# Performance work log

Hardware: AMD Instinct MI355X
Metric: run time of the kernel (lower is better)

Reference implementation:

```python
import jax, jax.numpy as jnp
import numpy as np

N = 50000      # batch_node_num (unique nodes)
E = 800000     # number of edges (avg degree 16)
IN = 128       # in_dim
OUT = 128      # out_dim
B = 10000      # query nodes


def setup_inputs() -> dict:
    key = jax.random.key(0)
    k = jax.random.split(key, 8)
    edges = jax.random.randint(k[0], (E, 2), 0, N, dtype=jnp.int64)
    node_idx = jax.random.randint(k[1], (B,), 0, N, dtype=jnp.int64)
    local_features = jax.random.normal(k[2], (N, IN), dtype=jnp.float32)
    W1 = jax.random.normal(k[3], (IN, OUT), dtype=jnp.float32) * (1.0 / np.sqrt(IN))
    b1 = jnp.zeros((OUT,), dtype=jnp.float32)
    W2 = jax.random.normal(k[4], (OUT, OUT), dtype=jnp.float32) * (1.0 / np.sqrt(OUT))
    b2 = jnp.zeros((OUT,), dtype=jnp.float32)
    return {"edges": edges, "node_idx": node_idx, "local_features": local_features,
            "W1": W1, "b1": b1, "W2": W2, "b2": b2, "ind": 2}


def reference(edges, node_idx, local_features, W1, b1, W2, b2, ind):
    mask = jnp.array([1.0, 1.0, 0.0, 0.0], dtype=jnp.float32)
    # Linear -> Tanh -> Linear (the out_linear_layer MLP)
    h = jnp.tanh(local_features @ W1 + b1) @ W2 + b2          # [N, OUT]
    src, dst = edges[:, 0], edges[:, 1]
    # self-loop edges get weight mask[ind], others weight 1
    values = jnp.where(src == dst, mask[ind], jnp.float32(1.0))  # [E]
    # spmm(matrix, ones) == per-row degree (weighted)
    row_sum = jax.ops.segment_sum(values, src, num_segments=N)   # [N]
    row_sum = jnp.where(row_sum == 0, jnp.float32(1.0), row_sum)
    # spmm(matrix, new_embeddings): gather dst embeddings, scatter-add to src
    results = jax.ops.segment_sum(values[:, None] * h[dst], src, num_segments=N)  # [N, OUT]
    output_emb = results / row_sum[:, None]
    return output_emb[node_idx]
```

## Files before the change

kernel.cpp:

```cpp
#include <hip/hip_runtime.h>

#define IN_DIM 128
#define CAP 128
#define LDT 136
#define SCAT_BLOCKS 384

typedef short v8s __attribute__((ext_vector_type(8)));
typedef float v4f __attribute__((ext_vector_type(4)));

__device__ inline unsigned short f2bf(float f) {
    unsigned int u = __float_as_uint(f);
    u += 0x7FFFu + ((u >> 16) & 1u);
    return (unsigned short)(u >> 16);
}
__device__ inline float bf2f(unsigned short h) {
    return __uint_as_float((unsigned int)h << 16);
}

__global__ __launch_bounds__(256) void prep(
    const float* __restrict__ W1, const float* __restrict__ W2,
    unsigned short* __restrict__ Wt1, unsigned short* __restrict__ Wt2,
    const int* __restrict__ node_idx, int* __restrict__ flag, int B,
    int* __restrict__ cursor, int N, int nbF)
{
    int bid = blockIdx.x;
    if (bid < 128) {
        int i = bid * 256 + threadIdx.x;
        int m = i >> 14, rem = i & 16383;
        int n = rem >> 7, k = rem & 127;
        float wv = (m ? W2 : W1)[k * 128 + n];
        int half = k >> 6, ch = (k >> 3) & 7, k0 = k & 7;
        int idx = half * 8192 + n * 64 + ((ch ^ (n & 7)) << 3) + k0;
        (m ? Wt2 : Wt1)[idx] = f2bf(wv);
    } else if (bid < 128 + nbF) {
        int i = (bid - 128) * 256 + threadIdx.x;
        if (i < B) flag[node_idx[i]] = 1;
    } else {
        int i = (bid - 128 - nbF) * 256 + threadIdx.x;
        if (i < N) cursor[i] = 0;
    }
}

__global__ __launch_bounds__(256, 3) void mlp_fill(
    const float* __restrict__ X,
    const unsigned short* __restrict__ Wt1, const unsigned short* __restrict__ Wt2,
    const float* __restrict__ b1, const float* __restrict__ b2,
    unsigned short* __restrict__ Hb, int nrows,
    const int* __restrict__ edges, const int* __restrict__ flag,
    const int* __restrict__ indp, int* __restrict__ cursor,
    unsigned short* __restrict__ col, int E, int mlpBlocks)
{
    const int bid = blockIdx.x;

    if (bid >= mlpBlocks) {
        const int keepSelf = (*indp < 2) ? 1 : 0;
        const int stride = SCAT_BLOCKS * 256;
        for (int e = (bid - mlpBlocks) * 256 + threadIdx.x; e < E; e += stride) {
            int2 ed = ((const int2*)edges)[e];
            if ((ed.x != ed.y || keepSelf) && flag[ed.x] == 1) {
                int p = atomicAdd(&cursor[ed.x], 1);
                if (p < CAP)
                    col[(size_t)ed.x * CAP + p] = (unsigned short)ed.y;
            }
        }
        return;
    }

    __shared__ uint4 Wl4[1024];
    __shared__ unsigned short Ts[4 * 32 * LDT];
    const unsigned short* Wls = (const unsigned short*)Wl4;
    const int t    = threadIdx.x;
    const int w    = t >> 6;
    const int lane = t & 63;
    const int l15  = lane & 15;
    const int quad = lane >> 4;
    const int R0   = bid * 128;
    const int wrow = w * 32;
    unsigned short* Tw = &Ts[w * 32 * LDT];

    int gr0 = R0 + wrow + l15;        gr0 = gr0 < nrows ? gr0 : nrows - 1;
    int gr1 = R0 + wrow + 16 + l15;   gr1 = gr1 < nrows ? gr1 : nrows - 1;
    const float* xrow[2] = { &X[(size_t)gr0 * 128 + quad * 8],
                             &X[(size_t)gr1 * 128 + quad * 8] };

    uint4 wreg[4];
#pragma unroll
    for (int j = 0; j < 4; ++j)
        wreg[j] = ((const uint4*)Wt1)[j * 256 + t];

    v4f acc[2][8];
#pragma unroll
    for (int rt = 0; rt < 2; ++rt)
#pragma unroll
        for (int ct = 0; ct < 8; ++ct)
            acc[rt][ct] = (v4f){0.f, 0.f, 0.f, 0.f};

#pragma unroll
    for (int j = 0; j < 4; ++j) Wl4[j * 256 + t] = wreg[j];
    __syncthreads();
#pragma unroll
    for (int j = 0; j < 4; ++j)
        wreg[j] = ((const uint4*)(Wt1 + 8192))[j * 256 + t];

#pragma unroll
    for (int kk = 0; kk < 4; ++kk) {
        if (kk == 2) {
            __syncthreads();
#pragma unroll
            for (int j = 0; j < 4; ++j) Wl4[j * 256 + t] = wreg[j];
            __syncthreads();
        }
        const int kk2 = kk & 1;
        v8s Bf[8];
#pragma unroll
        for (int ct = 0; ct < 8; ++ct)
            Bf[ct] = *(const v8s*)
                &Wls[(ct * 16 + l15) * 64 + ((((kk2 * 4 + quad)) ^ (l15 & 7)) << 3)];
        v8s Ar[2];
#pragma unroll
        for (int rt = 0; rt < 2; ++rt) {
            const float* xp = xrow[rt] + kk * 32;
            float4 x0 = *(const float4*)xp;
            float4 x1 = *(const float4*)(xp + 4);
            v8s av;
            av[0] = (short)f2bf(x0.x); av[1] = (short)f2bf(x0.y);
            av[2] = (short)f2bf(x0.z); av[3] = (short)f2bf(x0.w);
            av[4] = (short)f2bf(x1.x); av[5] = (short)f2bf(x1.y);
            av[6] = (short)f2bf(x1.z); av[7] = (short)f2bf(x1.w);
            Ar[rt] = av;
        }
#pragma unroll
        for (int ct = 0; ct < 8; ++ct)
#pragma unroll
            for (int rt = 0; rt < 2; ++rt)
                acc[rt][ct] = __builtin_amdgcn_mfma_f32_16x16x32_bf16(
                    Ar[rt], Bf[ct], acc[rt][ct], 0, 0, 0);
    }
#pragma unroll
    for (int ct = 0; ct < 8; ++ct) {
        float bias = b1[ct * 16 + l15];
#pragma unroll
        for (int rt = 0; rt < 2; ++rt) {
#pragma unroll
            for (int r = 0; r < 4; ++r)
                Tw[(rt * 16 + quad * 4 + r) * LDT + ct * 16 + l15] =
                    f2bf(tanhf(acc[rt][ct][r] + bias));
            acc[rt][ct] = (v4f){0.f, 0.f, 0.f, 0.f};
        }
    }
#pragma unroll
    for (int j = 0; j < 4; ++j)
        wreg[j] = ((const uint4*)Wt2)[j * 256 + t];
    __syncthreads();
#pragma unroll
    for (int j = 0; j < 4; ++j) Wl4[j * 256 + t] = wreg[j];
    __syncthreads();
#pragma unroll
    for (int j = 0; j < 4; ++j)
        wreg[j] = ((const uint4*)(Wt2 + 8192))[j * 256 + t];

#pragma unroll
    for (int kk = 0; kk < 4; ++kk) {
        if (kk == 2) {
            __syncthreads();
#pragma unroll
            for (int j = 0; j < 4; ++j) Wl4[j * 256 + t] = wreg[j];
            __syncthreads();
        }
        const int kk2 = kk & 1;
        v8s Bf[8];
#pragma unroll
        for (int ct = 0; ct < 8; ++ct)
            Bf[ct] = *(const v8s*)
                &Wls[(ct * 16 + l15) * 64 + ((((kk2 * 4 + quad)) ^ (l15 & 7)) << 3)];
        v8s Ar[2];
#pragma unroll
        for (int rt = 0; rt < 2; ++rt)
            Ar[rt] = *(const v8s*)
                &Tw[(rt * 16 + l15) * LDT + kk * 32 + quad * 8];
#pragma unroll
        for (int ct = 0; ct < 8; ++ct)
#pragma unroll
            for (int rt = 0; rt < 2; ++rt)
                acc[rt][ct] = __builtin_amdgcn_mfma_f32_16x16x32_bf16(
                    Ar[rt], Bf[ct], acc[rt][ct], 0, 0, 0);
    }
    asm volatile("s_waitcnt lgkmcnt(0)" ::: "memory");
#pragma unroll
    for (int ct = 0; ct < 8; ++ct) {
        float bias = b2[ct * 16 + l15];
#pragma unroll
        for (int rt = 0; rt < 2; ++rt)
#pragma unroll
            for (int r = 0; r < 4; ++r)
                Tw[(rt * 16 + quad * 4 + r) * LDT + ct * 16 + l15] =
                    f2bf(acc[rt][ct][r] + bias);
    }
    asm volatile("s_waitcnt lgkmcnt(0)" ::: "memory");
#pragma unroll
    for (int i = 0; i < 8; ++i) {
        int lr = i * 4 + quad;
        int c  = l15;
        uint4 v = *(const uint4*)&Tw[lr * LDT + c * 8];
        int grow = R0 + wrow + lr;
        if (grow < nrows)
            *(uint4*)&Hb[(size_t)grow * 128 + c * 8] = v;
    }
}

__global__ __launch_bounds__(256) void aggregate_out(
    const int* __restrict__ node_idx, const int* __restrict__ cursor,
    const unsigned short* __restrict__ col, const unsigned short* __restrict__ Hb,
    float* __restrict__ out, int B)
{
    int b = (int)((blockIdx.x * blockDim.x + threadIdx.x) >> 6);
    if (b >= B) return;
    int lane = threadIdx.x & 63;
    int v = node_idx[b];
    int deg = cursor[v];
    deg = deg < CAP ? deg : CAP;
    const unsigned short* cp = &col[(size_t)v * CAP];
    int myc = (lane < deg) ? (int)cp[lane] : 0;
    int dmax = deg < 64 ? deg : 64;
    float ax = 0.f, ay = 0.f, bx = 0.f, by = 0.f;
    int i = 0;
    for (; i + 1 < dmax; i += 2) {
        int d0 = __shfl(myc, i, 64);
        int d1 = __shfl(myc, i + 1, 64);
        unsigned int u0 = *(const unsigned int*)&Hb[(size_t)d0 * 128 + lane * 2];
        unsigned int u1 = *(const unsigned int*)&Hb[(size_t)d1 * 128 + lane * 2];
        ax += bf2f((unsigned short)(u0 & 0xFFFFu));
        ay += bf2f((unsigned short)(u0 >> 16));
        bx += bf2f((unsigned short)(u1 & 0xFFFFu));
        by += bf2f((unsigned short)(u1 >> 16));
    }
    if (i < dmax) {
        int d0 = __shfl(myc, i, 64);
        unsigned int u0 = *(const unsigned int*)&Hb[(size_t)d0 * 128 + lane * 2];
        ax += bf2f((unsigned short)(u0 & 0xFFFFu));
        ay += bf2f((unsigned short)(u0 >> 16));
    }
    for (int j = 64; j < deg; ++j) {
        int d0 = cp[j];
        unsigned int u0 = *(const unsigned int*)&Hb[(size_t)d0 * 128 + lane * 2];
        ax += bf2f((unsigned short)(u0 & 0xFFFFu));
        ay += bf2f((unsigned short)(u0 >> 16));
    }
    float den = (deg > 0) ? (float)deg : 1.0f;
    *(float2*)&out[(size_t)b * 128 + lane * 2] =
        make_float2((ax + bx) / den, (ay + by) / den);
}

extern "C" void kernel_launch(void* const* d_in, const int* in_sizes, int n_in,
                              void* d_out, int out_size, void* d_ws, size_t ws_size,
                              hipStream_t stream)
{
    const int*   edges    = (const int*)d_in[0];
    const int*   node_idx = (const int*)d_in[1];
    const float* X        = (const float*)d_in[2];
    const float* W1       = (const float*)d_in[3];
    const float* b1       = (const float*)d_in[4];
    const float* W2       = (const float*)d_in[5];
    const float* b2       = (const float*)d_in[6];
    const int*   indp     = (const int*)d_in[7];

    const int E = in_sizes[0] / 2;
    const int B = in_sizes[1];
    const int N = in_sizes[2] / IN_DIM;
    const int mlpBlocks = (N + 127) / 128;
    const int nbF = (B + 255) / 256;
    const int nbC = (N + 255) / 256;

    char* ws = (char*)d_ws;
    size_t off = 0;
    int* cursor = (int*)(ws + off); off += (size_t)N * 4;
    int* flag   = (int*)(ws + off); off += (size_t)N * 4;
    off = (off + 15) & ~(size_t)15;
    unsigned short* Hb  = (unsigned short*)(ws + off); off += (size_t)N * IN_DIM * 2;
    unsigned short* col = (unsigned short*)(ws + off); off += (size_t)N * CAP * 2;
    unsigned short* Wt1 = (unsigned short*)(ws + off); off += 16384 * 2;
    unsigned short* Wt2 = (unsigned short*)(ws + off); off += 16384 * 2;

    hipLaunchKernelGGL(prep, dim3(128 + nbF + nbC), dim3(256), 0, stream,
                       W1, W2, Wt1, Wt2, node_idx, flag, B, cursor, N, nbF);
    hipLaunchKernelGGL(mlp_fill, dim3(mlpBlocks + SCAT_BLOCKS), dim3(256),
                       0, stream, X, Wt1, Wt2, b1, b2, Hb, N,
                       edges, flag, indp, cursor, col, E, mlpBlocks);
    hipLaunchKernelGGL(aggregate_out, dim3((B * 64 + 255) / 256), dim3(256), 0,
                       stream, node_idx, cursor, col, Hb, (float*)d_out, B);
}
```

Before: 128.4 us.

## Fuse prep, MLP/scatter and aggregation into one cooperative persistent kernel

Replaces the three kernel launches with a single cooperative kernel that separates the phases with grid-wide syncs. A persistent grid (at most 768 blocks, sized by occupancy) loops over MLP tiles on one subset of blocks and runs the edge scatter on the rest, then all blocks do the aggregation. This removes launch gaps and inter-kernel drain time. In exchange it adds two grid barriers, loses parallelism because MLP tiles are now processed serially per block, and runs a host-side occupancy and device-property query on every launch.

```diff
diff --git a/kernel.cpp b/kernel.cpp
--- a/kernel.cpp
+++ b/kernel.cpp
@@ -1,9 +1,11 @@
 #include <hip/hip_runtime.h>
+#include <hip/hip_cooperative_groups.h>
+
+namespace cg = cooperative_groups;
 
 #define IN_DIM 128
 #define CAP 128
 #define LDT 136
-#define SCAT_BLOCKS 384
 
 typedef short v8s __attribute__((ext_vector_type(8)));
 typedef float v4f __attribute__((ext_vector_type(4)));
@@ -17,45 +19,184 @@
     return __uint_as_float((unsigned int)h << 16);
 }
 
-__global__ __launch_bounds__(256) void prep(
-    const float* __restrict__ W1, const float* __restrict__ W2,
+__global__ __launch_bounds__(256, 3) void mega(
+    const float* __restrict__ X, const float* __restrict__ W1,
+    const float* __restrict__ b1, const float* __restrict__ W2,
+    const float* __restrict__ b2, const int* __restrict__ edges,
+    const int* __restrict__ node_idx, const int* __restrict__ indp,
     unsigned short* __restrict__ Wt1, unsigned short* __restrict__ Wt2,
-    const int* __restrict__ node_idx, int* __restrict__ flag, int B,
-    int* __restrict__ cursor, int N, int nbF)
+    int* __restrict__ flag, int* __restrict__ cursor,
+    unsigned short* __restrict__ Hb, unsigned short* __restrict__ col,
+    float* __restrict__ out,
+    int E, int B, int N, int mlpB, int nTiles)
 {
-    int bid = blockIdx.x;
-    if (bid < 128) {
-        int i = bid * 256 + threadIdx.x;
+    cg::grid_group grid = cg::this_grid();
+    const int G = (int)gridDim.x;
+    const int t = threadIdx.x;
+    const int gtid = (int)blockIdx.x * 256 + t;
+    const int gstride = G * 256;
+
+    __shared__ uint4 Wl4[1024];
+    __shared__ unsigned short Ts[4 * 32 * LDT];
+
+    for (int i = gtid; i < 2 * IN_DIM * IN_DIM; i += gstride) {
         int m = i >> 14, rem = i & 16383;
         int n = rem >> 7, k = rem & 127;
         float wv = (m ? W2 : W1)[k * 128 + n];
         int half = k >> 6, ch = (k >> 3) & 7, k0 = k & 7;
         int idx = half * 8192 + n * 64 + ((ch ^ (n & 7)) << 3) + k0;
         (m ? Wt2 : Wt1)[idx] = f2bf(wv);
-    } else if (bid < 128 + nbF) {
-        int i = (bid - 128) * 256 + threadIdx.x;
-        if (i < B) flag[node_idx[i]] = 1;
+    }
+    for (int i = gtid; i < B; i += gstride) flag[node_idx[i]] = 1;
+    for (int i = gtid; i < N; i += gstride) cursor[i] = 0;
+
+    grid.sync();
+
+    const int w    = t >> 6;
+    const int lane = t & 63;
+    const int l15  = lane & 15;
+    const int quad = lane >> 4;
+
+    if ((int)blockIdx.x < mlpB) {
+        unsigned short* Tw = &Ts[w * 32 * LDT];
+        const unsigned short* Wls = (const unsigned short*)Wl4;
+        const int wrow = w * 32;
+        for (int tile = (int)blockIdx.x; tile < nTiles; tile += mlpB) {
+            __syncthreads();
+            const int R0 = tile * 128;
+            int gr0 = R0 + wrow + l15;        gr0 = gr0 < N ? gr0 : N - 1;
+            int gr1 = R0 + wrow + 16 + l15;   gr1 = gr1 < N ? gr1 : N - 1;
+            const float* xrow[2] = { &X[(size_t)gr0 * 128 + quad * 8],
+                                     &X[(size_t)gr1 * 128 + quad * 8] };
+
+            uint4 wreg[4];
+#pragma unroll
+            for (int j = 0; j < 4; ++j)
+                wreg[j] = ((const uint4*)Wt1)[j * 256 + t];
+
+            v4f acc[2][8];
+#pragma unroll
+            for (int rt = 0; rt < 2; ++rt)
+#pragma unroll
+                for (int ct = 0; ct < 8; ++ct)
+                    acc[rt][ct] = (v4f){0.f, 0.f, 0.f, 0.f};
+
+#pragma unroll
+            for (int j = 0; j < 4; ++j) Wl4[j * 256 + t] = wreg[j];
+            __syncthreads();
+#pragma unroll
+            for (int j = 0; j < 4; ++j)
+                wreg[j] = ((const uint4*)(Wt1 + 8192))[j * 256 + t];
+
+#pragma unroll
+            for (int kk = 0; kk < 4; ++kk) {
+                if (kk == 2) {
+                    __syncthreads();
+#pragma unroll
+                    for (int j = 0; j < 4; ++j) Wl4[j * 256 + t] = wreg[j];
+                    __syncthreads();
+                }
+                const int kk2 = kk & 1;
+                v8s Bf[8];
+#pragma unroll
+                for (int ct = 0; ct < 8; ++ct)
+                    Bf[ct] = *(const v8s*)
+                        &Wls[(ct * 16 + l15) * 64 + ((((kk2 * 4 + quad)) ^ (l15 & 7)) << 3)];
+                v8s Ar[2];
+#pragma unroll
+                for (int rt = 0; rt < 2; ++rt) {
+                    const float* xp = xrow[rt] + kk * 32;
+                    float4 x0 = *(const float4*)xp;
+                    float4 x1 = *(const float4*)(xp + 4);
+                    v8s av;
+                    av[0] = (short)f2bf(x0.x); av[1] = (short)f2bf(x0.y);
+                    av[2] = (short)f2bf(x0.z); av[3] = (short)f2bf(x0.w);
+                    av[4] = (short)f2bf(x1.x); av[5] = (short)f2bf(x1.y);
+                    av[6] = (short)f2bf(x1.z); av[7] = (short)f2bf(x1.w);
+                    Ar[rt] = av;
+                }
+#pragma unroll
+                for (int ct = 0; ct < 8; ++ct)
+#pragma unroll
+                    for (int rt = 0; rt < 2; ++rt)
+                        acc[rt][ct] = __builtin_amdgcn_mfma_f32_16x16x32_bf16(
+                            Ar[rt], Bf[ct], acc[rt][ct], 0, 0, 0);
+            }
+#pragma unroll
+            for (int ct = 0; ct < 8; ++ct) {
+                float bias = b1[ct * 16 + l15];
+#pragma unroll
+                for (int rt = 0; rt < 2; ++rt) {
+#pragma unroll
+                    for (int r = 0; r < 4; ++r)
+                        Tw[(rt * 16 + quad * 4 + r) * LDT + ct * 16 + l15] =
+                            f2bf(tanhf(acc[rt][ct][r] + bias));
+                    acc[rt][ct] = (v4f){0.f, 0.f, 0.f, 0.f};
+                }
+            }
+#pragma unroll
+            for (int j = 0; j < 4; ++j)
+                wreg[j] = ((const uint4*)Wt2)[j * 256 + t];
+            __syncthreads();
+#pragma unroll
+            for (int j = 0; j < 4; ++j) Wl4[j * 256 + t] = wreg[j];
+            __syncthreads();
+#pragma unroll
+            for (int j = 0; j < 4; ++j)
+                wreg[j] = ((const uint4*)(Wt2 + 8192))[j * 256 + t];
+
+#pragma unroll
+            for (int kk = 0; kk < 4; ++kk) {
+                if (kk == 2) {
+                    __syncthreads();
+#pragma unroll
+                    for (int j = 0; j < 4; ++j) Wl4[j * 256 + t] = wreg[j];
+                    __syncthreads();
+                }
+                const int kk2 = kk & 1;
+                v8s Bf[8];
+#pragma unroll
+                for (int ct = 0; ct < 8; ++ct)
+                    Bf[ct] = *(const v8s*)
+                        &Wls[(ct * 16 + l15) * 64 + ((((kk2 * 4 + quad)) ^ (l15 & 7)) << 3)];
+                v8s Ar[2];
+#pragma unroll
+                for (int rt = 0; rt < 2; ++rt)
+                    Ar[rt] = *(const v8s*)
+                        &Tw[(rt * 16 + l15) * LDT + kk * 32 + quad * 8];
+#pragma unroll
+                for (int ct = 0; ct < 8; ++ct)
+#pragma unroll
+                    for (int rt = 0; rt < 2; ++rt)
+                        acc[rt][ct] = __builtin_amdgcn_mfma_f32_16x16x32_bf16(
+                            Ar[rt], Bf[ct], acc[rt][ct], 0, 0, 0);
+            }
+            asm volatile("s_waitcnt lgkmcnt(0)" ::: "memory");
+#pragma unroll
+            for (int ct = 0; ct < 8; ++ct) {
+                float bias = b2[ct * 16 + l15];
+#pragma unroll
+                for (int rt = 0; rt < 2; ++rt)
+#pragma unroll
+                    for (int r = 0; r < 4; ++r)
+                        Tw[(rt * 16 + quad * 4 + r) * LDT + ct * 16 + l15] =
+                            f2bf(acc[rt][ct][r] + bias);
+            }
+            asm volatile("s_waitcnt lgkmcnt(0)" ::: "memory");
+#pragma unroll
+            for (int i = 0; i < 8; ++i) {
+                int lr = i * 4 + quad;
+                int c  = l15;
+                uint4 v = *(const uint4*)&Tw[lr * LDT + c * 8];
+                int grow = R0 + wrow + lr;
+                if (grow < N)
+                    *(uint4*)&Hb[(size_t)grow * 128 + c * 8] = v;
+            }
+        }
     } else {
-        int i = (bid - 128 - nbF) * 256 + threadIdx.x;
-        if (i < N) cursor[i] = 0;
-    }
-}
-
-__global__ __launch_bounds__(256, 3) void mlp_fill(
-    const float* __restrict__ X,
-    const unsigned short* __restrict__ Wt1, const unsigned short* __restrict__ Wt2,
-    const float* __restrict__ b1, const float* __restrict__ b2,
-    unsigned short* __restrict__ Hb, int nrows,
-    const int* __restrict__ edges, const int* __restrict__ flag,
-    const int* __restrict__ indp, int* __restrict__ cursor,
-    unsigned short* __restrict__ col, int E, int mlpBlocks)
-{
-    const int bid = blockIdx.x;
-
-    if (bid >= mlpBlocks) {
         const int keepSelf = (*indp < 2) ? 1 : 0;
-        const int stride = SCAT_BLOCKS * 256;
-        for (int e = (bid - mlpBlocks) * 256 + threadIdx.x; e < E; e += stride) {
+        const int scatB = G - mlpB;
+        for (int e = ((int)blockIdx.x - mlpB) * 256 + t; e < E; e += scatB * 256) {
             int2 ed = ((const int2*)edges)[e];
             if ((ed.x != ed.y || keepSelf) && flag[ed.x] == 1) {
                 int p = atomicAdd(&cursor[ed.x], 1);
@@ -63,192 +204,45 @@
                     col[(size_t)ed.x * CAP + p] = (unsigned short)ed.y;
             }
         }
-        return;
     }
 
-    __shared__ uint4 Wl4[1024];
-    __shared__ unsigned short Ts[4 * 32 * LDT];
-    const unsigned short* Wls = (const unsigned short*)Wl4;
-    const int t    = threadIdx.x;
-    const int w    = t >> 6;
-    const int lane = t & 63;
-    const int l15  = lane & 15;
-    const int quad = lane >> 4;
-    const int R0   = bid * 128;
-    const int wrow = w * 32;
-    unsigned short* Tw = &Ts[w * 32 * LDT];
-
-    int gr0 = R0 + wrow + l15;        gr0 = gr0 < nrows ? gr0 : nrows - 1;
-    int gr1 = R0 + wrow + 16 + l15;   gr1 = gr1 < nrows ? gr1 : nrows - 1;
-    const float* xrow[2] = { &X[(size_t)gr0 * 128 + quad * 8],
-                             &X[(size_t)gr1 * 128 + quad * 8] };
-
-    uint4 wreg[4];
-#pragma unroll
-    for (int j = 0; j < 4; ++j)
-        wreg[j] = ((const uint4*)Wt1)[j * 256 + t];
-
-    v4f acc[2][8];
-#pragma unroll
-    for (int rt = 0; rt < 2; ++rt)
-#pragma unroll
-        for (int ct = 0; ct < 8; ++ct)
-            acc[rt][ct] = (v4f){0.f, 0.f, 0.f, 0.f};
-
-#pragma unroll
-    for (int j = 0; j < 4; ++j) Wl4[j * 256 + t] = wreg[j];
-    __syncthreads();
-#pragma unroll
-    for (int j = 0; j < 4; ++j)
-        wreg[j] = ((const uint4*)(Wt1 + 8192))[j * 256 + t];
-
-#pragma unroll
-    for (int kk = 0; kk < 4; ++kk) {
-        if (kk == 2) {
-            __syncthreads();
-#pragma unroll
-            for (int j = 0; j < 4; ++j) Wl4[j * 256 + t] = wreg[j];
-            __syncthreads();
-        }
-        const int kk2 = kk & 1;
-        v8s Bf[8];
-#pragma unroll
-        for (int ct = 0; ct < 8; ++ct)
-            Bf[ct] = *(const v8s*)
-                &Wls[(ct * 16 + l15) * 64 + ((((kk2 * 4 + quad)) ^ (l15 & 7)) << 3)];
-        v8s Ar[2];
-#pragma unroll
-        for (int rt = 0; rt < 2; ++rt) {
-            const float* xp = xrow[rt] + kk * 32;
-            float4 x0 = *(const float4*)xp;
-            float4 x1 = *(const float4*)(xp + 4);
-            v8s av;
-            av[0] = (short)f2bf(x0.x); av[1] = (short)f2bf(x0.y);
-            av[2] = (short)f2bf(x0.z); av[3] = (short)f2bf(x0.w);
-            av[4] = (short)f2bf(x1.x); av[5] = (short)f2bf(x1.y);
-            av[6] = (short)f2bf(x1.z); av[7] = (short)f2bf(x1.w);
-            Ar[rt] = av;
-        }
-#pragma unroll
-        for (int ct = 0; ct < 8; ++ct)
-#pragma unroll
-            for (int rt = 0; rt < 2; ++rt)
-                acc[rt][ct] = __builtin_amdgcn_mfma_f32_16x16x32_bf16(
-                    Ar[rt], Bf[ct], acc[rt][ct], 0, 0, 0);
+    grid.sync();
+
+    for (int b = (int)blockIdx.x * 4 + w; b < B; b += G * 4) {
+        int v = node_idx[b];
+        int deg = cursor[v];
+        deg = deg < CAP ? deg : CAP;
+        const unsigned short* cp = &col[(size_t)v * CAP];
+        int myc = (lane < deg) ? (int)cp[lane] : 0;
+        int dmax = deg < 64 ? deg : 64;
+        float ax = 0.f, ay = 0.f, bx = 0.f, by = 0.f;
+        int i = 0;
+        for (; i + 1 < dmax; i += 2) {
+            int d0 = __shfl(myc, i, 64);
+            int d1 = __shfl(myc, i + 1, 64);
+            unsigned int u0 = *(const unsigned int*)&Hb[(size_t)d0 * 128 + lane * 2];
+            unsigned int u1 = *(const unsigned int*)&Hb[(size_t)d1 * 128 + lane * 2];
+            ax += bf2f((unsigned short)(u0 & 0xFFFFu));
+            ay += bf2f((unsigned short)(u0 >> 16));
+            bx += bf2f((unsigned short)(u1 & 0xFFFFu));
+            by += bf2f((unsigned short)(u1 >> 16));
+        }
+        if (i < dmax) {
+            int d0 = __shfl(myc, i, 64);
+            unsigned int u0 = *(const unsigned int*)&Hb[(size_t)d0 * 128 + lane * 2];
+            ax += bf2f((unsigned short)(u0 & 0xFFFFu));
+            ay += bf2f((unsigned short)(u0 >> 16));
+        }
+        for (int j = 64; j < deg; ++j) {
+            int d0 = cp[j];
+            unsigned int u0 = *(const unsigned int*)&Hb[(size_t)d0 * 128 + lane * 2];
+            ax += bf2f((unsigned short)(u0 & 0xFFFFu));
+            ay += bf2f((unsigned short)(u0 >> 16));
+        }
+        float den = (deg > 0) ? (float)deg : 1.0f;
+        *(float2*)&out[(size_t)b * 128 + lane * 2] =
+            make_float2((ax + bx) / den, (ay + by) / den);
     }
-#pragma unroll
-    for (int ct = 0; ct < 8; ++ct) {
-        float bias = b1[ct * 16 + l15];
-#pragma unroll
-        for (int rt = 0; rt < 2; ++rt) {
-#pragma unroll
-            for (int r = 0; r < 4; ++r)
-                Tw[(rt * 16 + quad * 4 + r) * LDT + ct * 16 + l15] =
-                    f2bf(tanhf(acc[rt][ct][r] + bias));
-            acc[rt][ct] = (v4f){0.f, 0.f, 0.f, 0.f};
-        }
-    }
-#pragma unroll
-    for (int j = 0; j < 4; ++j)
-        wreg[j] = ((const uint4*)Wt2)[j * 256 + t];
-    __syncthreads();
-#pragma unroll
-    for (int j = 0; j < 4; ++j) Wl4[j * 256 + t] = wreg[j];
-    __syncthreads();
-#pragma unroll
-    for (int j = 0; j < 4; ++j)
-        wreg[j] = ((const uint4*)(Wt2 + 8192))[j * 256 + t];
-
-#pragma unroll
-    for (int kk = 0; kk < 4; ++kk) {
-        if (kk == 2) {
-            __syncthreads();
-#pragma unroll
-            for (int j = 0; j < 4; ++j) Wl4[j * 256 + t] = wreg[j];
-            __syncthreads();
-        }
-        const int kk2 = kk & 1;
-        v8s Bf[8];
-#pragma unroll
-        for (int ct = 0; ct < 8; ++ct)
-            Bf[ct] = *(const v8s*)
-                &Wls[(ct * 16 + l15) * 64 + ((((kk2 * 4 + quad)) ^ (l15 & 7)) << 3)];
-        v8s Ar[2];
-#pragma unroll
-        for (int rt = 0; rt < 2; ++rt)
-            Ar[rt] = *(const v8s*)
-                &Tw[(rt * 16 + l15) * LDT + kk * 32 + quad * 8];
-#pragma unroll
-        for (int ct = 0; ct < 8; ++ct)
-#pragma unroll
-            for (int rt = 0; rt < 2; ++rt)
-                acc[rt][ct] = __builtin_amdgcn_mfma_f32_16x16x32_bf16(
-                    Ar[rt], Bf[ct], acc[rt][ct], 0, 0, 0);
-    }
-    asm volatile("s_waitcnt lgkmcnt(0)" ::: "memory");
-#pragma unroll
-    for (int ct = 0; ct < 8; ++ct) {
-        float bias = b2[ct * 16 + l15];
-#pragma unroll
-        for (int rt = 0; rt < 2; ++rt)
-#pragma unroll
-            for (int r = 0; r < 4; ++r)
-                Tw[(rt * 16 + quad * 4 + r) * LDT + ct * 16 + l15] =
-                    f2bf(acc[rt][ct][r] + bias);
-    }
-    asm volatile("s_waitcnt lgkmcnt(0)" ::: "memory");
-#pragma unroll
-    for (int i = 0; i < 8; ++i) {
-        int lr = i * 4 + quad;
-        int c  = l15;
-        uint4 v = *(const uint4*)&Tw[lr * LDT + c * 8];
-        int grow = R0 + wrow + lr;
-        if (grow < nrows)
-            *(uint4*)&Hb[(size_t)grow * 128 + c * 8] = v;
-    }
-}
-
-__global__ __launch_bounds__(256) void aggregate_out(
-    const int* __restrict__ node_idx, const int* __restrict__ cursor,
-    const unsigned short* __restrict__ col, const unsigned short* __restrict__ Hb,
-    float* __restrict__ out, int B)
-{
-    int b = (int)((blockIdx.x * blockDim.x + threadIdx.x) >> 6);
-    if (b >= B) return;
-    int lane = threadIdx.x & 63;
-    int v = node_idx[b];
-    int deg = cursor[v];
-    deg = deg < CAP ? deg : CAP;
-    const unsigned short* cp = &col[(size_t)v * CAP];
-    int myc = (lane < deg) ? (int)cp[lane] : 0;
-    int dmax = deg < 64 ? deg : 64;
-    float ax = 0.f, ay = 0.f, bx = 0.f, by = 0.f;
-    int i = 0;
-    for (; i + 1 < dmax; i += 2) {
-        int d0 = __shfl(myc, i, 64);
-        int d1 = __shfl(myc, i + 1, 64);
-        unsigned int u0 = *(const unsigned int*)&Hb[(size_t)d0 * 128 + lane * 2];
-        unsigned int u1 = *(const unsigned int*)&Hb[(size_t)d1 * 128 + lane * 2];
-        ax += bf2f((unsigned short)(u0 & 0xFFFFu));
-        ay += bf2f((unsigned short)(u0 >> 16));
-        bx += bf2f((unsigned short)(u1 & 0xFFFFu));
-        by += bf2f((unsigned short)(u1 >> 16));
-    }
-    if (i < dmax) {
-        int d0 = __shfl(myc, i, 64);
-        unsigned int u0 = *(const unsigned int*)&Hb[(size_t)d0 * 128 + lane * 2];
-        ax += bf2f((unsigned short)(u0 & 0xFFFFu));
-        ay += bf2f((unsigned short)(u0 >> 16));
-    }
-    for (int j = 64; j < deg; ++j) {
-        int d0 = cp[j];
-        unsigned int u0 = *(const unsigned int*)&Hb[(size_t)d0 * 128 + lane * 2];
-        ax += bf2f((unsigned short)(u0 & 0xFFFFu));
-        ay += bf2f((unsigned short)(u0 >> 16));
-    }
-    float den = (deg > 0) ? (float)deg : 1.0f;
-    *(float2*)&out[(size_t)b * 128 + lane * 2] =
-        make_float2((ax + bx) / den, (ay + by) / den);
 }
 
 extern "C" void kernel_launch(void* const* d_in, const int* in_sizes, int n_in,
@@ -264,12 +258,10 @@
     const float* b2       = (const float*)d_in[6];
     const int*   indp     = (const int*)d_in[7];
 
-    const int E = in_sizes[0] / 2;
-    const int B = in_sizes[1];
-    const int N = in_sizes[2] / IN_DIM;
-    const int mlpBlocks = (N + 127) / 128;
-    const int nbF = (B + 255) / 256;
-    const int nbC = (N + 255) / 256;
+    int E = in_sizes[0] / 2;
+    int B = in_sizes[1];
+    int N = in_sizes[2] / IN_DIM;
+    int nTiles = (N + 127) / 128;
 
     char* ws = (char*)d_ws;
     size_t off = 0;
@@ -280,12 +272,34 @@
     unsigned short* col = (unsigned short*)(ws + off); off += (size_t)N * CAP * 2;
     unsigned short* Wt1 = (unsigned short*)(ws + off); off += 16384 * 2;
     unsigned short* Wt2 = (unsigned short*)(ws + off); off += 16384 * 2;
-
-    hipLaunchKernelGGL(prep, dim3(128 + nbF + nbC), dim3(256), 0, stream,
-                       W1, W2, Wt1, Wt2, node_idx, flag, B, cursor, N, nbF);
-    hipLaunchKernelGGL(mlp_fill, dim3(mlpBlocks + SCAT_BLOCKS), dim3(256),
-                       0, stream, X, Wt1, Wt2, b1, b2, Hb, N,
-                       edges, flag, indp, cursor, col, E, mlpBlocks);
-    hipLaunchKernelGGL(aggregate_out, dim3((B * 64 + 255) / 256), dim3(256), 0,
-                       stream, node_idx, cursor, col, Hb, (float*)d_out, B);
+    float* outp = (float*)d_out;
+
+    int G = 768;
+    int occ = 0;
+    if (hipOccupancyMaxActiveBlocksPerMultiprocessor(
+            &occ, (const void*)mega, 256, 0) == hipSuccess && occ > 0) {
+        int dev = 0;
+        hipGetDevice(&dev);
+        hipDeviceProp_t prop;
+        if (hipGetDeviceProperties(&prop, dev) == hipSuccess &&
+            prop.multiProcessorCount > 0)
+            G = occ * prop.multiProcessorCount;
+    }
+    if (G > 768) G = 768;
+    if (G < 2)   G = 2;
+    int mlpB = G - 377;
+    if (mlpB < G / 2)   mlpB = G / 2;
+    if (mlpB > nTiles)  mlpB = nTiles;
+    if (mlpB < 1)       mlpB = 1;
+    if (mlpB >= G)      mlpB = G - 1;
+
+    void* args[] = {
+        (void*)&X, (void*)&W1, (void*)&b1, (void*)&W2, (void*)&b2,
+        (void*)&edges, (void*)&node_idx, (void*)&indp,
+        (void*)&Wt1, (void*)&Wt2, (void*)&flag, (void*)&cursor,
+        (void*)&Hb, (void*)&col, (void*)&outp,
+        (void*)&E, (void*)&B, (void*)&N, (void*)&mlpB, (void*)&nTiles
+    };
+    hipLaunchCooperativeKernel((const void*)mega, dim3(G), dim3(256),
+                               args, 0, stream);
 }
```

New measurement: 276.2 us. +115.1%, slower.
